# Optimization experiments

Hardware: AMD Instinct MI355X
Metric: run time of the kernel (lower is better)

## Reference

```python
import jax, jax.numpy as jnp
import numpy as np

N_NODES = 100000
N_EDGES = 1600000
D_FEAT = 64


def setup_inputs() -> dict:
    key = jax.random.key(0)
    k1, k2, k3, k4 = jax.random.split(key, 4)
    rows = jax.random.randint(k1, (N_EDGES,), 0, N_NODES, dtype=jnp.int32)
    cols = jax.random.randint(k2, (N_EDGES,), 0, N_NODES, dtype=jnp.int32)
    # nonnegative edge weights, like a normalized adjacency
    vals = jax.random.uniform(k3, (N_EDGES,), dtype=jnp.float32)
    embeds = jax.random.normal(k4, (N_NODES, D_FEAT), dtype=jnp.float32)
    return {"rows": rows, "cols": cols, "vals": vals, "embeds": embeds}


def reference(rows, cols, vals, embeds):
    # SpMM: out[r] = sum_{e: rows[e]==r} vals[e] * embeds[cols[e]]
    gathered = embeds[cols] * vals[:, None]        # [E, d]
    out = jax.ops.segment_sum(gathered, rows, num_segments=embeds.shape[0])  # [N, d]
    return out
```

## Files before the change

### kernel.cpp

```cpp
#include <hip/hip_runtime.h>

#define D_FEAT 64
#define NN 100000
#define SBROWS 512
#define NSB ((NN + SBROWS - 1) / SBROWS)
#define CAP 10240
#define BATCH 4096
#define OFFP (SBROWS + 1)

__device__ inline ushort f2bf(float f) {
    unsigned u = __float_as_uint(f);
    return (ushort)((u + 0x7FFFu + ((u >> 16) & 1u)) >> 16);
}
__global__ void fused_prep(const float* __restrict__ embeds, ushort* __restrict__ e16,
                           int n4, int* __restrict__ ccursors) {
    if (blockIdx.x == 0 && threadIdx.x < NSB) ccursors[threadIdx.x] = threadIdx.x * CAP;
    int i = blockIdx.x * blockDim.x + threadIdx.x;
    int stride = gridDim.x * blockDim.x;
    for (; i < n4; i += stride) {
        float4 f = ((const float4*)embeds)[i];
        ushort4 u;
        u.x = f2bf(f.x); u.y = f2bf(f.y); u.z = f2bf(f.z); u.w = f2bf(f.w);
        ((ushort4*)e16)[i] = u;
    }
}

__global__ void __launch_bounds__(512) coarse_split(const int* __restrict__ rows,
                                                    const int* __restrict__ cols,
                                                    const float* __restrict__ vals,
                                                    int* __restrict__ ccursors,
                                                    int2* __restrict__ tmp, int E) {
    __shared__ int2 pay[BATCH];
    __shared__ int hist[NSB], scanv[NSB], lcur[NSB], gbase[NSB], wlim[NSB];
    __shared__ int tsum[256];

    int b0 = blockIdx.x * BATCH;
    int n = E - b0; if (n > BATCH) n = BATCH;
    int t = threadIdx.x;

    for (int i = t; i < NSB; i += 512) hist[i] = 0;
    __syncthreads();

    for (int k = t; k < n; k += 512)
        atomicAdd(&hist[rows[b0 + k] >> 9], 1);
    __syncthreads();

    if (t < 256) tsum[t] = (t < NSB) ? hist[t] : 0;
    __syncthreads();
    for (int off = 1; off < 256; off <<= 1) {
        int x = 0;
        if (t < 256 && t >= off) x = tsum[t - off];
        __syncthreads();
        if (t < 256) tsum[t] += x;
        __syncthreads();
    }
    if (t < NSB) {
        int excl = (t > 0) ? tsum[t - 1] : 0;
        scanv[t] = excl;
        lcur[t]  = excl;
        int cnt = hist[t];
        int gb  = atomicAdd(&ccursors[t], cnt);
        int lim = t * CAP + CAP;
        int wl  = lim - gb; if (wl < 0) wl = 0; if (wl > cnt) wl = cnt;
        gbase[t] = gb; wlim[t] = wl;
    }
    __syncthreads();

    for (int k = t; k < n; k += 512) {
        int r  = rows[b0 + k];
        int sb = r >> 9;
        int idx = atomicAdd(&lcur[sb], 1);
        pay[idx] = make_int2(cols[b0 + k] | ((r & 511) << 17), __float_as_int(vals[b0 + k]));
    }
    __syncthreads();

    int wv = t >> 6, ln = t & 63;
    for (int s = wv; s < NSB; s += 8) {
        int sv = scanv[s], gb = gbase[s], wl = wlim[s];
        for (int j = ln; j < wl; j += 64) tmp[gb + j] = pay[sv + j];
    }
}

__global__ void __launch_bounds__(1024) fine_split(const int2* __restrict__ tmp,
                                                   const int* __restrict__ ccursors,
                                                   int* __restrict__ offsets,
                                                   int2* __restrict__ sedges) {
    __shared__ int lhist[SBROWS], lbase[SBROWS], lcur[SBROWS], tt[SBROWS];
    int sb = blockIdx.x;
    int t = threadIdx.x;
    int cstart = sb * CAP;
    int cnt = ccursors[sb] - cstart; if (cnt > CAP) cnt = CAP;
    int cend = cstart + cnt;

    if (t < SBROWS) lhist[t] = 0;
    __syncthreads();

    for (int i = cstart + t; i < cend; i += 1024)
        atomicAdd(&lhist[(tmp[i].x >> 17) & 511], 1);
    __syncthreads();

    if (t < SBROWS) tt[t] = lhist[t];
    __syncthreads();
    for (int off = 1; off < SBROWS; off <<= 1) {
        int x = 0;
        if (t < SBROWS && t >= off) x = tt[t - off];
        __syncthreads();
        if (t < SBROWS) tt[t] += x;
        __syncthreads();
    }
    if (t < SBROWS) {
        int excl = (t > 0) ? tt[t - 1] : 0;
        lbase[t] = cstart + excl;
        lcur[t]  = 0;
        offsets[sb * OFFP + t] = cstart + excl;
    }
    if (t == 0) offsets[sb * OFFP + SBROWS] = cend;
    __syncthreads();

    for (int i = cstart + t; i < cend; i += 1024) {
        int2 p = tmp[i];
        int fl = (p.x >> 17) & 511;
        int pos = lbase[fl] + atomicAdd(&lcur[fl], 1);
        sedges[pos] = make_int2(p.x & 0x1FFFF, p.y);
    }
}

__global__ void __launch_bounds__(256) row_spmm(const int* __restrict__ offsets,
                                                const int2* __restrict__ sedges,
                                                const ushort* __restrict__ e16,
                                                float* __restrict__ out) {
    __shared__ int2 stage[4][64];
    int w    = threadIdx.x >> 6;
    int lane = threadIdx.x & 63;
    int r0   = (blockIdx.x * 4 + w) * 4;
    int sb   = r0 >> 9;
    int obase = sb * OFFP + (r0 & 511);

    #pragma unroll
    for (int k = 0; k < 4; k++) {
        int row = r0 + k;
        int s = offsets[obase + k], e = offsets[obase + k + 1];
        float acc = 0.f;
        for (int base = s; base < e; base += 64) {
            int idx = base + lane;
            int2 se = (idx < e) ? sedges[idx] : make_int2(0, 0);
            stage[w][lane] = se;
            int m = e - base; if (m > 64) m = 64;
            int nsub = (m + 15) >> 4;
            for (int sub = 0; sub < nsub; sub++) {
                #pragma unroll
                for (int jj = 0; jj < 16; jj++) {
                    int2  sv = stage[w][sub * 16 + jj];
                    float v  = __int_as_float(sv.y);
                    ushort g16 = e16[(sv.x << 6) + lane];
                    float g  = __uint_as_float(((unsigned)g16) << 16);
                    acc = fmaf(v, g, acc);
                }
            }
        }
        out[((size_t)row << 6) + lane] = acc;
    }
}

__global__ void spmm_atomic_kernel(const int* __restrict__ rows, const int* __restrict__ cols,
                                   const float* __restrict__ vals, const float* __restrict__ embeds,
                                   float* __restrict__ out, int n_edges) {
    long long t = (long long)blockIdx.x * blockDim.x + threadIdx.x;
    int e = (int)(t >> 4);
    int f4 = ((int)t & 15) * 4;
    if (e >= n_edges) return;
    int r = rows[e], c = cols[e];
    float v = vals[e];
    const float4 emb = *reinterpret_cast<const float4*>(&embeds[(long long)c * D_FEAT + f4]);
    float* o = &out[(long long)r * D_FEAT + f4];
    atomicAdd(o + 0, v * emb.x);
    atomicAdd(o + 1, v * emb.y);
    atomicAdd(o + 2, v * emb.z);
    atomicAdd(o + 3, v * emb.w);
}

extern "C" void kernel_launch(void* const* d_in, const int* in_sizes, int n_in,
                              void* d_out, int out_size, void* d_ws, size_t ws_size,
                              hipStream_t stream) {
    const int*   rows   = (const int*)d_in[0];
    const int*   cols   = (const int*)d_in[1];
    const float* vals   = (const float*)d_in[2];
    const float* embeds = (const float*)d_in[3];
    float*       out    = (float*)d_out;
    int E = in_sizes[0];

    size_t need = (size_t)NSB * CAP * 16 + (size_t)NN * D_FEAT * 2
                + ((size_t)NSB * OFFP + NSB) * 4;

    if (ws_size >= need && E <= NSB * CAP) {
        char* ws = (char*)d_ws;
        int2*   tmp     = (int2*)ws;        ws += (size_t)NSB * CAP * 8;
        int2*   sedges  = (int2*)ws;        ws += (size_t)NSB * CAP * 8;
        ushort* e16     = (ushort*)ws;      ws += (size_t)NN * D_FEAT * 2;
        int*    offsets = (int*)ws;         ws += (size_t)NSB * OFFP * 4;
        int*    ccursors= (int*)ws;

        fused_prep<<<2048, 256, 0, stream>>>(embeds, e16, NN * D_FEAT / 4, ccursors);

        int nb1 = (E + BATCH - 1) / BATCH;
        coarse_split<<<nb1, 512, 0, stream>>>(rows, cols, vals, ccursors, tmp, E);
        fine_split<<<NSB, 1024, 0, stream>>>(tmp, ccursors, offsets, sedges);

        row_spmm<<<NN / 16, 256, 0, stream>>>(offsets, sedges, e16, out);
    } else {
        hipMemsetAsync(d_out, 0, (size_t)out_size * sizeof(float), stream);
        long long total = (long long)E * 16;
        int block = 256;
        spmm_atomic_kernel<<<(int)((total + block - 1) / block), block, 0, stream>>>(
            rows, cols, vals, embeds, out, E);
    }
}
```

Baseline: 86.54 us.

## Fuse per-superblock fine sort with row SpMM using LDS-resident edges

Merges the fine_split and row_spmm kernels into one kernel per 512-row superblock. Each block sorts its edges into shared memory and then computes the output rows straight from that buffer. This drops the global sedges and offsets arrays, their write and read-back traffic, and one kernel launch. In exchange the roughly 82KB shared buffer limits each CU to one 1024-thread block, and only about 196 blocks are launched. Each wave also walks 32 rows serially with a shallow unroll, so there is less parallelism to hide gather latency.

Result: slower. 122.1 us (+41.1%).

```diff
diff --git a/kernel.cpp b/kernel.cpp
--- a/kernel.cpp
+++ b/kernel.cpp
@@ -6,7 +6,6 @@
 #define NSB ((NN + SBROWS - 1) / SBROWS)
 #define CAP 10240
 #define BATCH 4096
-#define OFFP (SBROWS + 1)
 
 __device__ inline ushort f2bf(float f) {
     unsigned u = __float_as_uint(f);
@@ -81,22 +80,22 @@
     }
 }
 
-__global__ void __launch_bounds__(1024) fine_split(const int2* __restrict__ tmp,
-                                                   const int* __restrict__ ccursors,
-                                                   int* __restrict__ offsets,
-                                                   int2* __restrict__ sedges) {
+__global__ void __launch_bounds__(1024) fused_sort_spmm(const int2* __restrict__ tmp,
+                                                        const int* __restrict__ ccursors,
+                                                        const ushort* __restrict__ e16,
+                                                        float* __restrict__ out) {
+    __shared__ int2 sedl[CAP + 8];
     __shared__ int lhist[SBROWS], lbase[SBROWS], lcur[SBROWS], tt[SBROWS];
     int sb = blockIdx.x;
     int t = threadIdx.x;
     int cstart = sb * CAP;
     int cnt = ccursors[sb] - cstart; if (cnt > CAP) cnt = CAP;
-    int cend = cstart + cnt;
 
     if (t < SBROWS) lhist[t] = 0;
     __syncthreads();
 
-    for (int i = cstart + t; i < cend; i += 1024)
-        atomicAdd(&lhist[(tmp[i].x >> 17) & 511], 1);
+    for (int i = t; i < cnt; i += 1024)
+        atomicAdd(&lhist[(tmp[cstart + i].x >> 17) & 511], 1);
     __syncthreads();
 
     if (t < SBROWS) tt[t] = lhist[t];
@@ -109,56 +108,39 @@
         __syncthreads();
     }
     if (t < SBROWS) {
-        int excl = (t > 0) ? tt[t - 1] : 0;
-        lbase[t] = cstart + excl;
+        lbase[t] = (t > 0) ? tt[t - 1] : 0;
         lcur[t]  = 0;
-        offsets[sb * OFFP + t] = cstart + excl;
     }
-    if (t == 0) offsets[sb * OFFP + SBROWS] = cend;
     __syncthreads();
 
-    for (int i = cstart + t; i < cend; i += 1024) {
-        int2 p = tmp[i];
+    for (int i = t; i < cnt; i += 1024) {
+        int2 p = tmp[cstart + i];
         int fl = (p.x >> 17) & 511;
         int pos = lbase[fl] + atomicAdd(&lcur[fl], 1);
-        sedges[pos] = make_int2(p.x & 0x1FFFF, p.y);
+        sedl[pos] = make_int2(p.x & 0x1FFFF, p.y);
     }
-}
+    if (t < 8) sedl[cnt + t] = make_int2(0, 0);
+    __syncthreads();
 
-__global__ void __launch_bounds__(256) row_spmm(const int* __restrict__ offsets,
-                                                const int2* __restrict__ sedges,
-                                                const ushort* __restrict__ e16,
-                                                float* __restrict__ out) {
-    __shared__ int2 stage[4][64];
-    int w    = threadIdx.x >> 6;
-    int lane = threadIdx.x & 63;
-    int r0   = (blockIdx.x * 4 + w) * 4;
-    int sb   = r0 >> 9;
-    int obase = sb * OFFP + (r0 & 511);
-
-    #pragma unroll
-    for (int k = 0; k < 4; k++) {
-        int row = r0 + k;
-        int s = offsets[obase + k], e = offsets[obase + k + 1];
+    int w = t >> 6, lane = t & 63;
+    int gr0 = sb * SBROWS + w * 32;
+    for (int k = 0; k < 32; k++) {
+        int grow = gr0 + k;
+        if (grow >= NN) break;
+        int r = (grow - sb * SBROWS);
+        int s = lbase[r], e = s + lhist[r];
         float acc = 0.f;
-        for (int base = s; base < e; base += 64) {
-            int idx = base + lane;
-            int2 se = (idx < e) ? sedges[idx] : make_int2(0, 0);
-            stage[w][lane] = se;
-            int m = e - base; if (m > 64) m = 64;
-            int nsub = (m + 15) >> 4;
-            for (int sub = 0; sub < nsub; sub++) {
-                #pragma unroll
-                for (int jj = 0; jj < 16; jj++) {
-                    int2  sv = stage[w][sub * 16 + jj];
-                    float v  = __int_as_float(sv.y);
-                    ushort g16 = e16[(sv.x << 6) + lane];
-                    float g  = __uint_as_float(((unsigned)g16) << 16);
-                    acc = fmaf(v, g, acc);
-                }
+        for (int j = s; j < e; j += 4) {
+            #pragma unroll
+            for (int q = 0; q < 4; q++) {
+                int idx = j + q;
+                int2 sv = sedl[idx];
+                float v = (idx < e) ? __int_as_float(sv.y) : 0.f;
+                ushort g16 = e16[(sv.x << 6) + lane];
+                acc = fmaf(v, __uint_as_float(((unsigned)g16) << 16), acc);
             }
         }
-        out[((size_t)row << 6) + lane] = acc;
+        out[((size_t)grow << 6) + lane] = acc;
     }
 }
 
@@ -189,24 +171,20 @@
     float*       out    = (float*)d_out;
     int E = in_sizes[0];
 
-    size_t need = (size_t)NSB * CAP * 16 + (size_t)NN * D_FEAT * 2
-                + ((size_t)NSB * OFFP + NSB) * 4;
+    size_t need = (size_t)NSB * CAP * 8 + (size_t)NN * D_FEAT * 2 + (size_t)NSB * 4;
 
     if (ws_size >= need && E <= NSB * CAP) {
         char* ws = (char*)d_ws;
         int2*   tmp     = (int2*)ws;        ws += (size_t)NSB * CAP * 8;
-        int2*   sedges  = (int2*)ws;        ws += (size_t)NSB * CAP * 8;
         ushort* e16     = (ushort*)ws;      ws += (size_t)NN * D_FEAT * 2;
-        int*    offsets = (int*)ws;         ws += (size_t)NSB * OFFP * 4;
         int*    ccursors= (int*)ws;
 
         fused_prep<<<2048, 256, 0, stream>>>(embeds, e16, NN * D_FEAT / 4, ccursors);
 
         int nb1 = (E + BATCH - 1) / BATCH;
         coarse_split<<<nb1, 512, 0, stream>>>(rows, cols, vals, ccursors, tmp, E);
-        fine_split<<<NSB, 1024, 0, stream>>>(tmp, ccursors, offsets, sedges);
 
-        row_spmm<<<NN / 16, 256, 0, stream>>>(offsets, sedges, e16, out);
+        fused_sort_spmm<<<NSB, 1024, 0, stream>>>(tmp, ccursors, e16, out);
     } else {
         hipMemsetAsync(d_out, 0, (size_t)out_size * sizeof(float), stream);
         long long total = (long long)E * 16;
```
